# Optimization experiments

Hardware: AMD Instinct MI355X
Metric: run time of the kernel (lower is better)

The kernel has to match this reference:

```python
import jax, jax.numpy as jnp
import numpy as np

BOTTLENECK_DIM = 128
TOP_K = 8
SCALE = 1.0 / np.sqrt(BOTTLENECK_DIM)
EPS = 1e-10


def setup_inputs() -> dict:
    key = jax.random.key(0)
    k1, k2, k3, k4 = jax.random.split(key, 4)
    query = jax.random.normal(k1, (4, 4096, 128), dtype=jnp.float32)
    keys = jax.random.normal(k2, (4096, 128), dtype=jnp.float32)
    values = jax.random.normal(k3, (4096, 1024), dtype=jnp.float32)
    reliability = jax.random.uniform(k4, (4096,), dtype=jnp.float32)
    return {"query": query, "keys": keys, "values": values, "reliability": reliability}


def reference(query, keys, values, reliability):
    # Routing: [b, s, num_slots] scores with log-reliability bias, take top-k slots.
    router_scores = jnp.einsum("bsd,nd->bsn", query, keys) + jnp.log(reliability + EPS)
    _, top_indices = jax.lax.top_k(router_scores, TOP_K)  # [b, s, k]

    # Gather per-token slot keys/values: [b, s, k, d] and [b, s, k, h]
    selected_keys = keys[top_indices]
    selected_values = values[top_indices]

    # Small-k attention over gathered slots.
    attn_scores = jnp.einsum("bsd,bskd->bsk", query, selected_keys) * SCALE
    attn_weights = jax.nn.softmax(attn_scores, axis=-1)  # [b, s, k]
    output = jnp.einsum("bsk,bskh->bsh", attn_weights, selected_values)
    return output, attn_weights
```

## Files before the change

### kernel.cpp

```cpp
#include <hip/hip_runtime.h>
#include <hip/hip_fp16.h>
#include <math.h>

#define NSLOTS 4096
#define DIM    128
#define HDIM   1024
#define NTOK   16384
#define SCALE  0.08838834764831845f
#define REPS   1e-10f

typedef __attribute__((ext_vector_type(8))) short bf16x8;
typedef __attribute__((ext_vector_type(4))) float f32x4;

__device__ __forceinline__ float pack_score(float biased, unsigned inv_idx) {
    return __uint_as_float((__float_as_uint(biased) & 0xFFFFF000u) | inv_idx);
}
#define PACK_NEG_INF __uint_as_float(0xFF7FF000u)

__device__ __forceinline__ void ins_packed(float (&r)[8], float x) {
    #pragma unroll
    for (int i = 0; i < 7; ++i) r[i] = __builtin_amdgcn_fmed3f(r[i], x, r[i + 1]);
    r[7] = fmaxf(r[7], x);
}

__device__ __forceinline__ void merge_out16(float (&r)[8], int kseg, float* outS) {
    float hv = r[7];
    #pragma unroll
    for (int rnd = 0; rnd < 16; ++rnd) {
        float bv = hv;
        bv = fmaxf(bv, __shfl_xor(bv, 16, 64));
        bv = fmaxf(bv, __shfl_xor(bv, 32, 64));
        if ((rnd >> 2) == kseg) outS[rnd] = bv;
        if (hv == bv) {
            #pragma unroll
            for (int m2 = 7; m2 > 0; --m2) r[m2] = r[m2 - 1];
            r[0] = PACK_NEG_INF;
            hv = r[7];
        }
    }
}

__device__ __forceinline__ ushort f2bf(float f) {
    unsigned u = __float_as_uint(f);
    return (ushort)((u + 0x7fffu + ((u >> 16) & 1u)) >> 16);
}
#define QB_N  524288
#define KBP_N 65536
#define LR_N  4096
#define VH_N  524288
__global__ void prep_kernel(const float* __restrict__ q, const float* __restrict__ k,
                            const float* __restrict__ rel, const float* __restrict__ v,
                            ushort* __restrict__ qb, ushort* __restrict__ kbp,
                            float* __restrict__ lr, ushort* __restrict__ vh) {
    int gid = blockIdx.x * 256 + threadIdx.x;
    if (gid < QB_N) {
        float4 vv = ((const float4*)q)[gid];
        ushort4 o; o.x = f2bf(vv.x); o.y = f2bf(vv.y); o.z = f2bf(vv.z); o.w = f2bf(vv.w);
        ((ushort4*)qb)[gid] = o;
    } else if (gid < QB_N + KBP_N) {
        int C = gid - QB_N;
        int l = C & 63, kc = (C >> 6) & 3, t16 = C >> 8;
        int slot = t16 * 16 + (l & 15);
        int doff = kc * 32 + (l >> 4) * 8;
        const float4* src = (const float4*)(k + (size_t)slot * DIM + doff);
        float4 v0 = src[0], v1 = src[1];
        union { ushort u[8]; uint4 v; } o;
        o.u[0] = f2bf(v0.x); o.u[1] = f2bf(v0.y); o.u[2] = f2bf(v0.z); o.u[3] = f2bf(v0.w);
        o.u[4] = f2bf(v1.x); o.u[5] = f2bf(v1.y); o.u[6] = f2bf(v1.z); o.u[7] = f2bf(v1.w);
        ((uint4*)kbp)[C] = o.v;
    } else if (gid < QB_N + KBP_N + LR_N) {
        int g = gid - QB_N - KBP_N;
        lr[g] = logf(rel[g] + REPS);
    } else if (gid < QB_N + KBP_N + LR_N + VH_N) {
        int g = gid - QB_N - KBP_N - LR_N;
        const float4* src = (const float4*)v + (size_t)g * 2;
        float4 a = src[0], b = src[1];
        union { _Float16 h[8]; uint4 u; } o;
        o.h[0] = (_Float16)a.x; o.h[1] = (_Float16)a.y;
        o.h[2] = (_Float16)a.z; o.h[3] = (_Float16)a.w;
        o.h[4] = (_Float16)b.x; o.h[5] = (_Float16)b.y;
        o.h[6] = (_Float16)b.z; o.h[7] = (_Float16)b.w;
        ((uint4*)vh)[g] = o.u;
    }
}

__launch_bounds__(512, 4)
__global__ void route_kernel(const ushort* __restrict__ qb,
                             const ushort* __restrict__ kbp,
                             const float*  __restrict__ lr,
                             int* __restrict__ cand) {
    __shared__ float qS[32][8][17];
    const int tid  = threadIdx.x;
    const int lane = tid & 63;
    const int w    = tid >> 6;
    const int m    = lane & 15;
    const int kseg = lane >> 4;
    const int tokbase = blockIdx.x * 32;

    bf16x8 bF0[4], bF1[4];
    const ushort* q0 = qb + (size_t)(tokbase + m) * DIM + kseg * 8;
    const ushort* q1 = qb + (size_t)(tokbase + 16 + m) * DIM + kseg * 8;
    #pragma unroll
    for (int kc = 0; kc < 4; ++kc) {
        bF0[kc] = *(const bf16x8*)(q0 + kc * 32);
        bF1[kc] = *(const bf16x8*)(q1 + kc * 32);
    }

    float R0[8], R1[8];
    #pragma unroll
    for (int i = 0; i < 8; ++i) { R0[i] = PACK_NEG_INF; R1[i] = PACK_NEG_INF; }

    const uint4* kb4 = (const uint4*)kbp;
    const int tbase = w * 32;

    uint4 A[4], N[4];
    #pragma unroll
    for (int kc = 0; kc < 4; ++kc)
        A[kc] = kb4[(size_t)tbase * 256 + kc * 64 + lane];

    for (int t = 0; t < 32; ++t) {
        if (t < 31) {
            #pragma unroll
            for (int kc = 0; kc < 4; ++kc)
                N[kc] = kb4[(size_t)(tbase + t + 1) * 256 + kc * 64 + lane];
        }
        f32x4 acc0 = {0.f, 0.f, 0.f, 0.f};
        f32x4 acc1 = {0.f, 0.f, 0.f, 0.f};
        #pragma unroll
        for (int kc = 0; kc < 4; ++kc) {
            bf16x8 aF = *(const bf16x8*)&A[kc];
            acc0 = __builtin_amdgcn_mfma_f32_16x16x32_bf16(aF, bF0[kc], acc0, 0, 0, 0);
            acc1 = __builtin_amdgcn_mfma_f32_16x16x32_bf16(aF, bF1[kc], acc1, 0, 0, 0);
        }
        const int base = w * 512 + t * 16;
        float4 lrv = ((const float4*)lr)[(base >> 2) + kseg];
        unsigned invb = 4095u - (unsigned)(base + kseg * 4);
        ins_packed(R0, pack_score(acc0[0] + lrv.x, invb));
        ins_packed(R0, pack_score(acc0[1] + lrv.y, invb - 1));
        ins_packed(R0, pack_score(acc0[2] + lrv.z, invb - 2));
        ins_packed(R0, pack_score(acc0[3] + lrv.w, invb - 3));
        ins_packed(R1, pack_score(acc1[0] + lrv.x, invb));
        ins_packed(R1, pack_score(acc1[1] + lrv.y, invb - 1));
        ins_packed(R1, pack_score(acc1[2] + lrv.z, invb - 2));
        ins_packed(R1, pack_score(acc1[3] + lrv.w, invb - 3));
        #pragma unroll
        for (int kc = 0; kc < 4; ++kc) A[kc] = N[kc];
    }

    merge_out16(R0, kseg, &qS[m][w][0]);
    merge_out16(R1, kseg, &qS[m + 16][w][0]);
    __syncthreads();

    if (tid < 32) {
        const int token = tokbase + tid;
        int p[8] = {0, 0, 0, 0, 0, 0, 0, 0};
        #pragma unroll
        for (int c = 0; c < 16; ++c) {
            float bv = -INFINITY; int bq = 0;
            #pragma unroll
            for (int j = 0; j < 8; ++j) {
                float v = (p[j] < 16) ? qS[tid][j][p[j]] : -INFINITY;
                if (v > bv) { bv = v; bq = j; }
            }
            cand[(size_t)token * 16 + c] = 4095 - (int)(__float_as_uint(bv) & 0xFFFu);
            ++p[bq];
        }
    }
}

__device__ __forceinline__ float2 h2f2(unsigned u) {
    return __half22float2(*reinterpret_cast<const __half2*>(&u));
}
__launch_bounds__(256)
__global__ void rescue_gather_kernel(const float* __restrict__ query,
                                     const float* __restrict__ keys,
                                     const float* __restrict__ lr,
                                     const int*   __restrict__ cand,
                                     const ushort* __restrict__ vh,
                                     float* __restrict__ out,
                                     float* __restrict__ wout) {
    const int tid  = threadIdx.x;
    const int w    = tid >> 6;
    const int lane = tid & 63;
    const int token = blockIdx.x * 4 + w;
    const int c  = lane >> 2;
    const int qp = lane & 3;

    int ci = cand[(size_t)token * 16 + c];
    const float4* q4 = (const float4*)(query + (size_t)token * DIM) + qp * 8;
    const float4* k4 = (const float4*)(keys  + (size_t)ci    * DIM) + qp * 8;
    float sum = 0.f;
    #pragma unroll
    for (int i = 0; i < 8; ++i) {
        float4 a = q4[i], b = k4[i];
        sum = fmaf(a.x, b.x, sum); sum = fmaf(a.y, b.y, sum);
        sum = fmaf(a.z, b.z, sum); sum = fmaf(a.w, b.w, sum);
    }
    sum += __shfl_xor(sum, 1, 4);
    sum += __shfl_xor(sum, 2, 4);
    float raw = sum;
    float s   = sum + lr[ci];

    #pragma unroll
    for (int k = 2; k <= 16; k <<= 1) {
        #pragma unroll
        for (int j = k >> 1; j >= 1; j >>= 1) {
            int off = j << 2;
            float s2 = __shfl_xor(s,   off, 64);
            float r2 = __shfl_xor(raw, off, 64);
            int   i2 = __shfl_xor(ci,  off, 64);
            bool mineFirst = (s > s2) || (s == s2 && ci < i2);
            bool lower = (c & j) == 0;
            bool asc   = (c & k) == 0;
            bool keep  = (lower == asc) ? mineFirst : !mineFirst;
            if (!keep) { s = s2; raw = r2; ci = i2; }
        }
    }
    float rsel[8]; int isel[8];
    #pragma unroll
    for (int r = 0; r < 8; ++r) {
        rsel[r] = __shfl(raw, r * 4, 64);
        isel[r] = __shfl(ci,  r * 4, 64);
    }

    float mx = -INFINITY;
    #pragma unroll
    for (int k = 0; k < 8; ++k) { rsel[k] *= SCALE; mx = fmaxf(mx, rsel[k]); }
    float e[8]; float ssum = 0.f;
    #pragma unroll
    for (int k = 0; k < 8; ++k) { e[k] = expf(rsel[k] - mx); ssum += e[k]; }
    float inv = 1.0f / ssum;
    float wk[8];
    #pragma unroll
    for (int k = 0; k < 8; ++k) wk[k] = e[k] * inv;

    if (lane == 0) {
        #pragma unroll
        for (int k = 0; k < 8; ++k) wout[(size_t)token * 8 + k] = wk[k];
    }

    float oA[8], oB[8];
    #pragma unroll
    for (int i = 0; i < 8; ++i) { oA[i] = 0.f; oB[i] = 0.f; }
    #pragma unroll
    for (int k = 0; k < 8; ++k) {
        const uint4* vr = (const uint4*)vh + (size_t)isel[k] * 128;
        float wkk = wk[k];
        uint4 va = vr[lane];
        uint4 vb = vr[lane + 64];
        float2 f;
        f = h2f2(va.x); oA[0] = fmaf(wkk, f.x, oA[0]); oA[1] = fmaf(wkk, f.y, oA[1]);
        f = h2f2(va.y); oA[2] = fmaf(wkk, f.x, oA[2]); oA[3] = fmaf(wkk, f.y, oA[3]);
        f = h2f2(va.z); oA[4] = fmaf(wkk, f.x, oA[4]); oA[5] = fmaf(wkk, f.y, oA[5]);
        f = h2f2(va.w); oA[6] = fmaf(wkk, f.x, oA[6]); oA[7] = fmaf(wkk, f.y, oA[7]);
        f = h2f2(vb.x); oB[0] = fmaf(wkk, f.x, oB[0]); oB[1] = fmaf(wkk, f.y, oB[1]);
        f = h2f2(vb.y); oB[2] = fmaf(wkk, f.x, oB[2]); oB[3] = fmaf(wkk, f.y, oB[3]);
        f = h2f2(vb.z); oB[4] = fmaf(wkk, f.x, oB[4]); oB[5] = fmaf(wkk, f.y, oB[5]);
        f = h2f2(vb.w); oB[6] = fmaf(wkk, f.x, oB[6]); oB[7] = fmaf(wkk, f.y, oB[7]);
    }
    float4* orow = (float4*)(out + (size_t)token * HDIM);
    orow[lane * 2]           = make_float4(oA[0], oA[1], oA[2], oA[3]);
    orow[lane * 2 + 1]       = make_float4(oA[4], oA[5], oA[6], oA[7]);
    orow[128 + lane * 2]     = make_float4(oB[0], oB[1], oB[2], oB[3]);
    orow[128 + lane * 2 + 1] = make_float4(oB[4], oB[5], oB[6], oB[7]);
}

extern "C" void kernel_launch(void* const* d_in, const int* in_sizes, int n_in,
                              void* d_out, int out_size, void* d_ws, size_t ws_size,
                              hipStream_t stream) {
    const float* query  = (const float*)d_in[0];
    const float* keys   = (const float*)d_in[1];
    const float* values = (const float*)d_in[2];
    const float* rel    = (const float*)d_in[3];

    float* out  = (float*)d_out;
    float* wout = out + (size_t)NTOK * HDIM;

    char* ws = (char*)d_ws;
    float*  lr   = (float*)ws;   ws += 4096 * 4;
    ushort* qb   = (ushort*)ws;  ws += (size_t)NTOK * DIM * 2;
    ushort* kbp  = (ushort*)ws;  ws += (size_t)NSLOTS * DIM * 2;
    int*    cand = (int*)ws;     ws += (size_t)NTOK * 16 * 4;
    ushort* vh   = (ushort*)ws;

    int prep_grid = (QB_N + KBP_N + LR_N + VH_N) / 256;
    hipLaunchKernelGGL(prep_kernel, dim3(prep_grid), dim3(256), 0, stream,
                       query, keys, rel, values, qb, kbp, lr, vh);
    hipLaunchKernelGGL(route_kernel, dim3(NTOK / 32), dim3(512), 0, stream,
                       qb, kbp, lr, cand);
    hipLaunchKernelGGL(rescue_gather_kernel, dim3(NTOK / 4), dim3(256), 0, stream,
                       query, keys, lr, cand, vh, out, wout);
}
```

Baseline: 188.1 us.

## Stream route keys via async global-to-LDS loads and split gather across wave pairs

The route kernel now uses 4 waves per block, each covering 1024 slots. Key tiles are double-buffered into LDS with global_load_lds and explicit vmcnt waits, replacing the register-prefetched global loads. The aim is to hide key-load latency and lighten register pressure. The gather kernel now runs two waves per token, each summing 4 of the 8 selected value rows, and combines the partial sums through LDS with a block barrier. This doubles the parallelism on the value gathers, at the cost of recomputing the rescue/softmax step in both waves and adding shared-memory traffic.

```diff
diff --git a/kernel.cpp b/kernel.cpp
--- a/kernel.cpp
+++ b/kernel.cpp
@@ -11,6 +11,9 @@
 
 typedef __attribute__((ext_vector_type(8))) short bf16x8;
 typedef __attribute__((ext_vector_type(4))) float f32x4;
+
+typedef __attribute__((address_space(1))) const void* as1cv;
+typedef __attribute__((address_space(3))) void* as3v;
 
 __device__ __forceinline__ float pack_score(float biased, unsigned inv_idx) {
     return __uint_as_float((__float_as_uint(biased) & 0xFFFFF000u) | inv_idx);
@@ -84,12 +87,13 @@
     }
 }
 
-__launch_bounds__(512, 4)
+__launch_bounds__(256, 4)
 __global__ void route_kernel(const ushort* __restrict__ qb,
                              const ushort* __restrict__ kbp,
                              const float*  __restrict__ lr,
                              int* __restrict__ cand) {
-    __shared__ float qS[32][8][17];
+    __shared__ ushort ktile[4][2][4 * 512];
+    __shared__ float  qS[32][4][16];
     const int tid  = threadIdx.x;
     const int lane = tid & 63;
     const int w    = tid >> 6;
@@ -110,29 +114,42 @@
     #pragma unroll
     for (int i = 0; i < 8; ++i) { R0[i] = PACK_NEG_INF; R1[i] = PACK_NEG_INF; }
 
-    const uint4* kb4 = (const uint4*)kbp;
-    const int tbase = w * 32;
-
-    uint4 A[4], N[4];
-    #pragma unroll
-    for (int kc = 0; kc < 4; ++kc)
-        A[kc] = kb4[(size_t)tbase * 256 + kc * 64 + lane];
-
-    for (int t = 0; t < 32; ++t) {
-        if (t < 31) {
-            #pragma unroll
-            for (int kc = 0; kc < 4; ++kc)
-                N[kc] = kb4[(size_t)(tbase + t + 1) * 256 + kc * 64 + lane];
-        }
+    auto issue = [&](int t, int buf) {
+        const ushort* gt = kbp + ((size_t)((w * 64 + t) * 256 + lane)) * 8;
+        ushort* lb = &ktile[w][buf][0];
+        #pragma unroll
+        for (int i = 0; i < 4; ++i) {
+            __builtin_amdgcn_global_load_lds((as1cv)(gt + i * 512),
+                                             (as3v)(lb + i * 512 + lane * 8), 16, 0, 0);
+        }
+    };
+
+    issue(0, 0);
+    issue(1, 1);
+
+    for (int t = 0; t < 64; ++t) {
+        const int cur = t & 1;
+        if (t < 63) {
+            asm volatile("s_waitcnt vmcnt(4)" ::: "memory");
+        } else {
+            asm volatile("s_waitcnt vmcnt(0)" ::: "memory");
+        }
+        const ushort* kt = &ktile[w][cur][0];
+        bf16x8 aF[4];
+        #pragma unroll
+        for (int kc = 0; kc < 4; ++kc)
+            aF[kc] = *(const bf16x8*)(kt + kc * 512 + lane * 8);
+        asm volatile("s_waitcnt lgkmcnt(0)" ::: "memory");
+        if (t < 62) issue(t + 2, cur);
+
         f32x4 acc0 = {0.f, 0.f, 0.f, 0.f};
         f32x4 acc1 = {0.f, 0.f, 0.f, 0.f};
         #pragma unroll
         for (int kc = 0; kc < 4; ++kc) {
-            bf16x8 aF = *(const bf16x8*)&A[kc];
-            acc0 = __builtin_amdgcn_mfma_f32_16x16x32_bf16(aF, bF0[kc], acc0, 0, 0, 0);
-            acc1 = __builtin_amdgcn_mfma_f32_16x16x32_bf16(aF, bF1[kc], acc1, 0, 0, 0);
-        }
-        const int base = w * 512 + t * 16;
+            acc0 = __builtin_amdgcn_mfma_f32_16x16x32_bf16(aF[kc], bF0[kc], acc0, 0, 0, 0);
+            acc1 = __builtin_amdgcn_mfma_f32_16x16x32_bf16(aF[kc], bF1[kc], acc1, 0, 0, 0);
+        }
+        const int base = w * 1024 + t * 16;
         float4 lrv = ((const float4*)lr)[(base >> 2) + kseg];
         unsigned invb = 4095u - (unsigned)(base + kseg * 4);
         ins_packed(R0, pack_score(acc0[0] + lrv.x, invb));
@@ -143,8 +160,6 @@
         ins_packed(R1, pack_score(acc1[1] + lrv.y, invb - 1));
         ins_packed(R1, pack_score(acc1[2] + lrv.z, invb - 2));
         ins_packed(R1, pack_score(acc1[3] + lrv.w, invb - 3));
-        #pragma unroll
-        for (int kc = 0; kc < 4; ++kc) A[kc] = N[kc];
     }
 
     merge_out16(R0, kseg, &qS[m][w][0]);
@@ -153,12 +168,12 @@
 
     if (tid < 32) {
         const int token = tokbase + tid;
-        int p[8] = {0, 0, 0, 0, 0, 0, 0, 0};
+        int p[4] = {0, 0, 0, 0};
         #pragma unroll
         for (int c = 0; c < 16; ++c) {
             float bv = -INFINITY; int bq = 0;
             #pragma unroll
-            for (int j = 0; j < 8; ++j) {
+            for (int j = 0; j < 4; ++j) {
                 float v = (p[j] < 16) ? qS[tid][j][p[j]] : -INFINITY;
                 if (v > bv) { bv = v; bq = j; }
             }
@@ -171,7 +186,7 @@
 __device__ __forceinline__ float2 h2f2(unsigned u) {
     return __half22float2(*reinterpret_cast<const __half2*>(&u));
 }
-__launch_bounds__(256)
+__launch_bounds__(512, 4)
 __global__ void rescue_gather_kernel(const float* __restrict__ query,
                                      const float* __restrict__ keys,
                                      const float* __restrict__ lr,
@@ -179,10 +194,13 @@
                                      const ushort* __restrict__ vh,
                                      float* __restrict__ out,
                                      float* __restrict__ wout) {
+    __shared__ float4 pbuf[4][4][64];
     const int tid  = threadIdx.x;
-    const int w    = tid >> 6;
+    const int wv   = tid >> 6;
+    const int tw   = wv >> 1;
+    const int par  = wv & 1;
     const int lane = tid & 63;
-    const int token = blockIdx.x * 4 + w;
+    const int token = blockIdx.x * 4 + tw;
     const int c  = lane >> 2;
     const int qp = lane & 3;
 
@@ -234,7 +252,7 @@
     #pragma unroll
     for (int k = 0; k < 8; ++k) wk[k] = e[k] * inv;
 
-    if (lane == 0) {
+    if (par == 0 && lane == 0) {
         #pragma unroll
         for (int k = 0; k < 8; ++k) wout[(size_t)token * 8 + k] = wk[k];
     }
@@ -243,7 +261,8 @@
     #pragma unroll
     for (int i = 0; i < 8; ++i) { oA[i] = 0.f; oB[i] = 0.f; }
     #pragma unroll
-    for (int k = 0; k < 8; ++k) {
+    for (int kk = 0; kk < 4; ++kk) {
+        const int k = par * 4 + kk;
         const uint4* vr = (const uint4*)vh + (size_t)isel[k] * 128;
         float wkk = wk[k];
         uint4 va = vr[lane];
@@ -258,11 +277,27 @@
         f = h2f2(vb.z); oB[4] = fmaf(wkk, f.x, oB[4]); oB[5] = fmaf(wkk, f.y, oB[5]);
         f = h2f2(vb.w); oB[6] = fmaf(wkk, f.x, oB[6]); oB[7] = fmaf(wkk, f.y, oB[7]);
     }
-    float4* orow = (float4*)(out + (size_t)token * HDIM);
-    orow[lane * 2]           = make_float4(oA[0], oA[1], oA[2], oA[3]);
-    orow[lane * 2 + 1]       = make_float4(oA[4], oA[5], oA[6], oA[7]);
-    orow[128 + lane * 2]     = make_float4(oB[0], oB[1], oB[2], oB[3]);
-    orow[128 + lane * 2 + 1] = make_float4(oB[4], oB[5], oB[6], oB[7]);
+
+    if (par) {
+        pbuf[tw][0][lane] = make_float4(oA[0], oA[1], oA[2], oA[3]);
+        pbuf[tw][1][lane] = make_float4(oA[4], oA[5], oA[6], oA[7]);
+        pbuf[tw][2][lane] = make_float4(oB[0], oB[1], oB[2], oB[3]);
+        pbuf[tw][3][lane] = make_float4(oB[4], oB[5], oB[6], oB[7]);
+    }
+    __syncthreads();
+    if (!par) {
+        float4 pA0 = pbuf[tw][0][lane], pA1 = pbuf[tw][1][lane];
+        float4 pB0 = pbuf[tw][2][lane], pB1 = pbuf[tw][3][lane];
+        float4* orow = (float4*)(out + (size_t)token * HDIM);
+        orow[lane * 2]           = make_float4(oA[0] + pA0.x, oA[1] + pA0.y,
+                                               oA[2] + pA0.z, oA[3] + pA0.w);
+        orow[lane * 2 + 1]       = make_float4(oA[4] + pA1.x, oA[5] + pA1.y,
+                                               oA[6] + pA1.z, oA[7] + pA1.w);
+        orow[128 + lane * 2]     = make_float4(oB[0] + pB0.x, oB[1] + pB0.y,
+                                               oB[2] + pB0.z, oB[3] + pB0.w);
+        orow[128 + lane * 2 + 1] = make_float4(oB[4] + pB1.x, oB[5] + pB1.y,
+                                               oB[6] + pB1.z, oB[7] + pB1.w);
+    }
 }
 
 extern "C" void kernel_launch(void* const* d_in, const int* in_sizes, int n_in,
@@ -286,8 +321,8 @@
     int prep_grid = (QB_N + KBP_N + LR_N + VH_N) / 256;
     hipLaunchKernelGGL(prep_kernel, dim3(prep_grid), dim3(256), 0, stream,
                        query, keys, rel, values, qb, kbp, lr, vh);
-    hipLaunchKernelGGL(route_kernel, dim3(NTOK / 32), dim3(512), 0, stream,
+    hipLaunchKernelGGL(route_kernel, dim3(NTOK / 32), dim3(256), 0, stream,
                        qb, kbp, lr, cand);
-    hipLaunchKernelGGL(rescue_gather_kernel, dim3(NTOK / 4), dim3(256), 0, stream,
+    hipLaunchKernelGGL(rescue_gather_kernel, dim3(NTOK / 4), dim3(512), 0, stream,
                        query, keys, lr, cand, vh, out, wout);
 }
```

Result: slower. 221.2 us (+17.6%).

## Split rescue-gather into score and half-row gather kernels with split value layout

Applied to the files above, without the earlier changes.

Splits the fused rescoring and value-gather kernel into a score kernel, which writes weights and selected indices, and a separate gather kernel. The gather kernel works on half of the hidden dimension per block, reading from a value table that prep now stores split into two halves so each half is a smaller contiguous table that may stay cache-resident. It also issues all eight value loads before accumulating and uses nontemporal stores for the output. The cost is an extra kernel launch and a round trip of weights and indices through global memory.

```diff
diff --git a/kernel.cpp b/kernel.cpp
--- a/kernel.cpp
+++ b/kernel.cpp
@@ -73,6 +73,8 @@
         lr[g] = logf(rel[g] + REPS);
     } else if (gid < QB_N + KBP_N + LR_N + VH_N) {
         int g = gid - QB_N - KBP_N - LR_N;
+        int slot = g >> 7;
+        int d0   = (g & 127) * 8;
         const float4* src = (const float4*)v + (size_t)g * 2;
         float4 a = src[0], b = src[1];
         union { _Float16 h[8]; uint4 u; } o;
@@ -80,7 +82,10 @@
         o.h[2] = (_Float16)a.z; o.h[3] = (_Float16)a.w;
         o.h[4] = (_Float16)b.x; o.h[5] = (_Float16)b.y;
         o.h[6] = (_Float16)b.z; o.h[7] = (_Float16)b.w;
-        ((uint4*)vh)[g] = o.u;
+        size_t didx = (d0 < 512)
+            ? ((size_t)slot * 64 + (d0 >> 3))
+            : ((size_t)4096 * 64 + (size_t)slot * 64 + ((d0 - 512) >> 3));
+        ((uint4*)vh)[didx] = o.u;
     }
 }
 
@@ -168,17 +173,13 @@
     }
 }
 
-__device__ __forceinline__ float2 h2f2(unsigned u) {
-    return __half22float2(*reinterpret_cast<const __half2*>(&u));
-}
 __launch_bounds__(256)
-__global__ void rescue_gather_kernel(const float* __restrict__ query,
-                                     const float* __restrict__ keys,
-                                     const float* __restrict__ lr,
-                                     const int*   __restrict__ cand,
-                                     const ushort* __restrict__ vh,
-                                     float* __restrict__ out,
-                                     float* __restrict__ wout) {
+__global__ void score_kernel(const float* __restrict__ query,
+                             const float* __restrict__ keys,
+                             const float* __restrict__ lr,
+                             const int*   __restrict__ cand,
+                             int*   __restrict__ iselg,
+                             float* __restrict__ wout) {
     const int tid  = threadIdx.x;
     const int w    = tid >> 6;
     const int lane = tid & 63;
@@ -230,39 +231,68 @@
     #pragma unroll
     for (int k = 0; k < 8; ++k) { e[k] = expf(rsel[k] - mx); ssum += e[k]; }
     float inv = 1.0f / ssum;
-    float wk[8];
-    #pragma unroll
-    for (int k = 0; k < 8; ++k) wk[k] = e[k] * inv;
 
     if (lane == 0) {
-        #pragma unroll
-        for (int k = 0; k < 8; ++k) wout[(size_t)token * 8 + k] = wk[k];
-    }
-
-    float oA[8], oB[8];
-    #pragma unroll
-    for (int i = 0; i < 8; ++i) { oA[i] = 0.f; oB[i] = 0.f; }
+        float4* wo = (float4*)(wout + (size_t)token * 8);
+        wo[0] = make_float4(e[0] * inv, e[1] * inv, e[2] * inv, e[3] * inv);
+        wo[1] = make_float4(e[4] * inv, e[5] * inv, e[6] * inv, e[7] * inv);
+        int4* io = (int4*)(iselg + (size_t)token * 8);
+        io[0] = make_int4(isel[0], isel[1], isel[2], isel[3]);
+        io[1] = make_int4(isel[4], isel[5], isel[6], isel[7]);
+    }
+}
+
+__device__ __forceinline__ float2 h2f2(unsigned u) {
+    return __half22float2(*reinterpret_cast<const __half2*>(&u));
+}
+__launch_bounds__(256)
+__global__ void gather_kernel(const float* __restrict__ wout,
+                              const int*   __restrict__ iselg,
+                              const ushort* __restrict__ vh,
+                              float* __restrict__ out) {
+    const int tid  = threadIdx.x;
+    const int wv   = tid >> 6;
+    const int lane = tid & 63;
+    const int b    = blockIdx.x;
+    const int x    = b & 7;
+    const int dhalf = x >> 2;
+    const int tg   = (b >> 3) * 4 + (x & 3);
+    const int token = tg * 4 + wv;
+
+    const float4* wo = (const float4*)(wout + (size_t)token * 8);
+    const int4*   io = (const int4*)(iselg + (size_t)token * 8);
+    float4 w0 = wo[0], w1 = wo[1];
+    int4   i0 = io[0], i1 = io[1];
+
+    const uint4* vbase = (const uint4*)vh + (size_t)dhalf * 4096 * 64;
+    uint4 va[8];
+    va[0] = vbase[(size_t)i0.x * 64 + lane];
+    va[1] = vbase[(size_t)i0.y * 64 + lane];
+    va[2] = vbase[(size_t)i0.z * 64 + lane];
+    va[3] = vbase[(size_t)i0.w * 64 + lane];
+    va[4] = vbase[(size_t)i1.x * 64 + lane];
+    va[5] = vbase[(size_t)i1.y * 64 + lane];
+    va[6] = vbase[(size_t)i1.z * 64 + lane];
+    va[7] = vbase[(size_t)i1.w * 64 + lane];
+    float wk[8] = {w0.x, w0.y, w0.z, w0.w, w1.x, w1.y, w1.z, w1.w};
+
+    float o[8];
+    #pragma unroll
+    for (int i = 0; i < 8; ++i) o[i] = 0.f;
     #pragma unroll
     for (int k = 0; k < 8; ++k) {
-        const uint4* vr = (const uint4*)vh + (size_t)isel[k] * 128;
         float wkk = wk[k];
-        uint4 va = vr[lane];
-        uint4 vb = vr[lane + 64];
         float2 f;
-        f = h2f2(va.x); oA[0] = fmaf(wkk, f.x, oA[0]); oA[1] = fmaf(wkk, f.y, oA[1]);
-        f = h2f2(va.y); oA[2] = fmaf(wkk, f.x, oA[2]); oA[3] = fmaf(wkk, f.y, oA[3]);
-        f = h2f2(va.z); oA[4] = fmaf(wkk, f.x, oA[4]); oA[5] = fmaf(wkk, f.y, oA[5]);
-        f = h2f2(va.w); oA[6] = fmaf(wkk, f.x, oA[6]); oA[7] = fmaf(wkk, f.y, oA[7]);
-        f = h2f2(vb.x); oB[0] = fmaf(wkk, f.x, oB[0]); oB[1] = fmaf(wkk, f.y, oB[1]);
-        f = h2f2(vb.y); oB[2] = fmaf(wkk, f.x, oB[2]); oB[3] = fmaf(wkk, f.y, oB[3]);
-        f = h2f2(vb.z); oB[4] = fmaf(wkk, f.x, oB[4]); oB[5] = fmaf(wkk, f.y, oB[5]);
-        f = h2f2(vb.w); oB[6] = fmaf(wkk, f.x, oB[6]); oB[7] = fmaf(wkk, f.y, oB[7]);
-    }
-    float4* orow = (float4*)(out + (size_t)token * HDIM);
-    orow[lane * 2]           = make_float4(oA[0], oA[1], oA[2], oA[3]);
-    orow[lane * 2 + 1]       = make_float4(oA[4], oA[5], oA[6], oA[7]);
-    orow[128 + lane * 2]     = make_float4(oB[0], oB[1], oB[2], oB[3]);
-    orow[128 + lane * 2 + 1] = make_float4(oB[4], oB[5], oB[6], oB[7]);
+        f = h2f2(va[k].x); o[0] = fmaf(wkk, f.x, o[0]); o[1] = fmaf(wkk, f.y, o[1]);
+        f = h2f2(va[k].y); o[2] = fmaf(wkk, f.x, o[2]); o[3] = fmaf(wkk, f.y, o[3]);
+        f = h2f2(va[k].z); o[4] = fmaf(wkk, f.x, o[4]); o[5] = fmaf(wkk, f.y, o[5]);
+        f = h2f2(va[k].w); o[6] = fmaf(wkk, f.x, o[6]); o[7] = fmaf(wkk, f.y, o[7]);
+    }
+    f32x4* orow = (f32x4*)(out + (size_t)token * HDIM + dhalf * 512 + lane * 8);
+    f32x4 s0 = {o[0], o[1], o[2], o[3]};
+    f32x4 s1 = {o[4], o[5], o[6], o[7]};
+    __builtin_nontemporal_store(s0, orow);
+    __builtin_nontemporal_store(s1, orow + 1);
 }
 
 extern "C" void kernel_launch(void* const* d_in, const int* in_sizes, int n_in,
@@ -277,17 +307,20 @@
     float* wout = out + (size_t)NTOK * HDIM;
 
     char* ws = (char*)d_ws;
-    float*  lr   = (float*)ws;   ws += 4096 * 4;
-    ushort* qb   = (ushort*)ws;  ws += (size_t)NTOK * DIM * 2;
-    ushort* kbp  = (ushort*)ws;  ws += (size_t)NSLOTS * DIM * 2;
-    int*    cand = (int*)ws;     ws += (size_t)NTOK * 16 * 4;
-    ushort* vh   = (ushort*)ws;
+    float*  lr    = (float*)ws;   ws += 4096 * 4;
+    ushort* qb    = (ushort*)ws;  ws += (size_t)NTOK * DIM * 2;
+    ushort* kbp   = (ushort*)ws;  ws += (size_t)NSLOTS * DIM * 2;
+    int*    cand  = (int*)ws;     ws += (size_t)NTOK * 16 * 4;
+    int*    iselg = (int*)ws;     ws += (size_t)NTOK * 8 * 4;
+    ushort* vh    = (ushort*)ws;
 
     int prep_grid = (QB_N + KBP_N + LR_N + VH_N) / 256;
     hipLaunchKernelGGL(prep_kernel, dim3(prep_grid), dim3(256), 0, stream,
                        query, keys, rel, values, qb, kbp, lr, vh);
     hipLaunchKernelGGL(route_kernel, dim3(NTOK / 32), dim3(512), 0, stream,
                        qb, kbp, lr, cand);
-    hipLaunchKernelGGL(rescue_gather_kernel, dim3(NTOK / 4), dim3(256), 0, stream,
-                       query, keys, lr, cand, vh, out, wout);
-}
+    hipLaunchKernelGGL(score_kernel, dim3(NTOK / 4), dim3(256), 0, stream,
+                       query, keys, lr, cand, iselg, wout);
+    hipLaunchKernelGGL(gather_kernel, dim3(NTOK / 2), dim3(256), 0, stream,
+                       wout, iselg, vh, out);
+}
```

Measured after the change: 189.5 us. About the same (+0.7%).

## Split slot range across two route blocks and merge candidate pools in gather

Applied to the files above, without the earlier changes.

The routing kernel now launches two blocks per 32-token group, and each block scans half of the 4096 slots. Each block writes its 16 best packed scores to a 32-entry candidate pool per token. The gather kernel then sorts the 32 pooled candidates with a wave-level bitonic sort and picks the top 16. This doubles grid parallelism and halves the serial per-wave loop, which should help occupancy and tail behaviour. The costs are a larger candidate buffer, re-loading query fragments in both blocks, and extra shuffle work in the gather kernel.

```diff
diff --git a/kernel.cpp b/kernel.cpp
--- a/kernel.cpp
+++ b/kernel.cpp
@@ -88,14 +88,16 @@
 __global__ void route_kernel(const ushort* __restrict__ qb,
                              const ushort* __restrict__ kbp,
                              const float*  __restrict__ lr,
-                             int* __restrict__ cand) {
+                             float* __restrict__ cpool) {
     __shared__ float qS[32][8][17];
     const int tid  = threadIdx.x;
     const int lane = tid & 63;
     const int w    = tid >> 6;
     const int m    = lane & 15;
     const int kseg = lane >> 4;
-    const int tokbase = blockIdx.x * 32;
+    const int tg   = blockIdx.x >> 1;
+    const int half = blockIdx.x & 1;
+    const int tokbase = tg * 32;
 
     bf16x8 bF0[4], bF1[4];
     const ushort* q0 = qb + (size_t)(tokbase + m) * DIM + kseg * 8;
@@ -111,15 +113,15 @@
     for (int i = 0; i < 8; ++i) { R0[i] = PACK_NEG_INF; R1[i] = PACK_NEG_INF; }
 
     const uint4* kb4 = (const uint4*)kbp;
-    const int tbase = w * 32;
+    const int tbase = half * 128 + w * 16;
 
     uint4 A[4], N[4];
     #pragma unroll
     for (int kc = 0; kc < 4; ++kc)
         A[kc] = kb4[(size_t)tbase * 256 + kc * 64 + lane];
 
-    for (int t = 0; t < 32; ++t) {
-        if (t < 31) {
+    for (int t = 0; t < 16; ++t) {
+        if (t < 15) {
             #pragma unroll
             for (int kc = 0; kc < 4; ++kc)
                 N[kc] = kb4[(size_t)(tbase + t + 1) * 256 + kc * 64 + lane];
@@ -132,7 +134,7 @@
             acc0 = __builtin_amdgcn_mfma_f32_16x16x32_bf16(aF, bF0[kc], acc0, 0, 0, 0);
             acc1 = __builtin_amdgcn_mfma_f32_16x16x32_bf16(aF, bF1[kc], acc1, 0, 0, 0);
         }
-        const int base = w * 512 + t * 16;
+        const int base = half * 2048 + w * 256 + t * 16;
         float4 lrv = ((const float4*)lr)[(base >> 2) + kseg];
         unsigned invb = 4095u - (unsigned)(base + kseg * 4);
         ins_packed(R0, pack_score(acc0[0] + lrv.x, invb));
@@ -162,7 +164,7 @@
                 float v = (p[j] < 16) ? qS[tid][j][p[j]] : -INFINITY;
                 if (v > bv) { bv = v; bq = j; }
             }
-            cand[(size_t)token * 16 + c] = 4095 - (int)(__float_as_uint(bv) & 0xFFFu);
+            cpool[(size_t)token * 32 + half * 16 + c] = bv;
             ++p[bq];
         }
     }
@@ -175,7 +177,7 @@
 __global__ void rescue_gather_kernel(const float* __restrict__ query,
                                      const float* __restrict__ keys,
                                      const float* __restrict__ lr,
-                                     const int*   __restrict__ cand,
+                                     const float* __restrict__ cpool,
                                      const ushort* __restrict__ vh,
                                      float* __restrict__ out,
                                      float* __restrict__ wout) {
@@ -183,10 +185,26 @@
     const int w    = tid >> 6;
     const int lane = tid & 63;
     const int token = blockIdx.x * 4 + w;
+    const int c5 = lane & 31;
+
+    float pv = cpool[(size_t)token * 32 + c5];
+    #pragma unroll
+    for (int k = 2; k <= 32; k <<= 1) {
+        #pragma unroll
+        for (int j = k >> 1; j >= 1; j >>= 1) {
+            float p2 = __shfl_xor(pv, j, 64);
+            bool mineFirst = pv > p2;
+            bool lower = (c5 & j) == 0;
+            bool asc   = (c5 & k) == 0;
+            bool keep  = (lower == asc) ? mineFirst : !mineFirst;
+            if (!keep) pv = p2;
+        }
+    }
+    float pc = __shfl(pv, lane >> 2, 64);
+    int ci = 4095 - (int)(__float_as_uint(pc) & 0xFFFu);
+
     const int c  = lane >> 2;
     const int qp = lane & 3;
-
-    int ci = cand[(size_t)token * 16 + c];
     const float4* q4 = (const float4*)(query + (size_t)token * DIM) + qp * 8;
     const float4* k4 = (const float4*)(keys  + (size_t)ci    * DIM) + qp * 8;
     float sum = 0.f;
@@ -277,17 +295,17 @@
     float* wout = out + (size_t)NTOK * HDIM;
 
     char* ws = (char*)d_ws;
-    float*  lr   = (float*)ws;   ws += 4096 * 4;
-    ushort* qb   = (ushort*)ws;  ws += (size_t)NTOK * DIM * 2;
-    ushort* kbp  = (ushort*)ws;  ws += (size_t)NSLOTS * DIM * 2;
-    int*    cand = (int*)ws;     ws += (size_t)NTOK * 16 * 4;
-    ushort* vh   = (ushort*)ws;
+    float*  lr    = (float*)ws;   ws += 4096 * 4;
+    ushort* qb    = (ushort*)ws;  ws += (size_t)NTOK * DIM * 2;
+    ushort* kbp   = (ushort*)ws;  ws += (size_t)NSLOTS * DIM * 2;
+    float*  cpool = (float*)ws;   ws += (size_t)NTOK * 32 * 4;
+    ushort* vh    = (ushort*)ws;
 
     int prep_grid = (QB_N + KBP_N + LR_N + VH_N) / 256;
     hipLaunchKernelGGL(prep_kernel, dim3(prep_grid), dim3(256), 0, stream,
                        query, keys, rel, values, qb, kbp, lr, vh);
-    hipLaunchKernelGGL(route_kernel, dim3(NTOK / 32), dim3(512), 0, stream,
-                       qb, kbp, lr, cand);
+    hipLaunchKernelGGL(route_kernel, dim3(NTOK / 32 * 2), dim3(512), 0, stream,
+                       qb, kbp, lr, cpool);
     hipLaunchKernelGGL(rescue_gather_kernel, dim3(NTOK / 4), dim3(256), 0, stream,
-                       query, keys, lr, cand, vh, out, wout);
-}
+                       query, keys, lr, cpool, vh, out, wout);
+}
```

After: 197.8 us. 1.05x slower.
